# Optimization experiments

Measured on AMD Instinct MI355X. Metric: run time of the kernel, lower is better.

The kernel has to match this reference:

```python
import jax, jax.numpy as jnp
import numpy as np

N_NODES = 512      # nodes in the original graph
N_SUB = 512        # NodeDeleted -> one subgraph per node
E_SUB = 2097152    # edges in the union-of-subgraphs graph (avg degree 8)
E_ORIG = 8192      # edges in the original graph
IN_DIM = 64
EMB = 64
L = 4
TASKS = 10


def setup_inputs() -> dict:
    key = jax.random.key(0)
    ks = jax.random.split(key, 16)
    NT = N_NODES * N_SUB
    x = jax.random.normal(ks[0], (NT, IN_DIM), jnp.float32)
    # edges stay within a subgraph: global id = subgraph_id * N + local id
    eg = jax.random.randint(ks[1], (E_SUB,), 0, N_SUB)
    src = jax.random.randint(ks[2], (E_SUB,), 0, N_NODES)
    dst = jax.random.randint(ks[3], (E_SUB,), 0, N_NODES)
    edge_index = jnp.stack([eg * N_NODES + src, eg * N_NODES + dst]).astype(jnp.int32)
    original_edge_index = jax.random.randint(ks[4], (2, E_ORIG), 0, N_NODES).astype(jnp.int32)
    subgraph_node_idx = jnp.tile(jnp.arange(N_NODES, dtype=jnp.int32), N_SUB)
    subgraph_batch = jnp.repeat(jnp.arange(N_SUB, dtype=jnp.int32), N_NODES)
    p = lambda k, shape: jax.random.normal(k, shape, jnp.float32) * 0.05
    return dict(
        x=x,
        Wrel=p(ks[5], (L, EMB, IN_DIM)), brel=jnp.zeros((L, EMB), jnp.float32),
        Wroot=p(ks[6], (L, EMB, IN_DIM)),
        bn_gamma=jnp.ones((L, EMB), jnp.float32), bn_beta=jnp.zeros((L, EMB), jnp.float32),
        Wrel_s=p(ks[7], (L, EMB, IN_DIM)), brel_s=jnp.zeros((L, EMB), jnp.float32),
        Wroot_s=p(ks[8], (L, EMB, IN_DIM)),
        bns_gamma=jnp.ones((L, EMB), jnp.float32), bns_beta=jnp.zeros((L, EMB), jnp.float32),
        W1=p(ks[9], (2 * EMB, EMB)), b1=jnp.zeros((2 * EMB,), jnp.float32),
        W2=p(ks[10], (TASKS, 2 * EMB)), b2=jnp.zeros((TASKS,), jnp.float32),
        edge_index=edge_index, original_edge_index=original_edge_index,
        subgraph_node_idx=subgraph_node_idx, subgraph_batch=subgraph_batch,
        num_nodes_int=N_NODES,
    )


def _gconv(h, ei, Wr, br, Wt, n):
    # PyG GraphConv, aggr='add': lin_rel(sum_{j->i} x_j) + lin_root(x_i)
    agg = jax.ops.segment_sum(h[ei[0]], ei[1], num_segments=n)
    return agg @ Wr.T + br + h @ Wt.T


def _bn(h, g, b):
    # BatchNorm1d, training mode: biased batch stats, eps=1e-5
    mu = h.mean(0)
    var = ((h - mu) ** 2).mean(0)
    return (h - mu) * jax.lax.rsqrt(var + 1e-5) * g + b


def _smean(src, idx, n):
    s = jax.ops.segment_sum(src, idx, num_segments=n)
    c = jax.ops.segment_sum(jnp.ones((src.shape[0], 1), src.dtype), idx, num_segments=n)
    return s / jnp.maximum(c, 1.0)


def reference(x, Wrel, brel, Wroot, bn_gamma, bn_beta, Wrel_s, brel_s, Wroot_s,
              bns_gamma, bns_beta, W1, b1, W2, b2,
              edge_index, original_edge_index, subgraph_node_idx, subgraph_batch,
              num_nodes_int):
    N = num_nodes_int
    NT = x.shape[0]
    S = NT // N  # num_subgraphs
    h = x
    for i in range(Wrel.shape[0]):
        h1 = _bn(_gconv(h, edge_index, Wrel[i], brel[i], Wroot[i], NT),
                 bn_gamma[i], bn_beta[i])
        x_sum = _smean(h, subgraph_node_idx, N)              # [N, emb]
        h2 = _bn(_gconv(x_sum, original_edge_index, Wrel_s[i], brel_s[i], Wroot_s[i], N),
                 bns_gamma[i], bns_beta[i])
        h = jax.nn.relu(h1 + jnp.tile(h2, (S, 1)))           # broadcast h2 to every subgraph
    x_nodes = _smean(h, subgraph_node_idx, N)                # [N, emb]
    z = jax.nn.log_softmax(x_nodes, axis=-1)                 # log_softmax BEFORE final MLP (as in source)
    out = jax.nn.relu(z @ W1.T + b1) @ W2.T + b2             # [N, num_tasks]
    return out
```

## Files before the change

### kernel.cpp

```cpp
#include <hip/hip_runtime.h>
#include <math.h>

#define NT 262144
#define NS 512
#define ES 2097152
#define EO 8192
#define NLAYER 4
#define WROW 68
#define BSL 704
#define EREG 8192

typedef short bf16x8 __attribute__((ext_vector_type(8)));
typedef float f32x4 __attribute__((ext_vector_type(4)));

__device__ __forceinline__ void cvt_hilo(const float* v, bf16x8* hi, bf16x8* lo) {
    union U { bf16x8 v; unsigned u[4]; };
    U H, L;
    #pragma unroll
    for (int q = 0; q < 4; q++) {
        float v0 = v[2 * q], v1 = v[2 * q + 1];
        unsigned h01;
        asm("v_cvt_pk_bf16_f32 %0, %1, %2" : "=v"(h01) : "v"(v0), "v"(v1));
        float l0 = v0 - __uint_as_float(h01 << 16);
        float l1 = v1 - __uint_as_float(h01 & 0xffff0000u);
        unsigned l01;
        asm("v_cvt_pk_bf16_f32 %0, %1, %2" : "=v"(l01) : "v"(l0), "v"(l1));
        H.u[q] = h01; L.u[q] = l01;
    }
    *hi = H.v; *lo = L.v;
}

__global__ __launch_bounds__(256) void bucket_kernel(const int* __restrict__ ei,
        int* __restrict__ gcur, unsigned* __restrict__ rbuf) {
    __shared__ int lcnt[512];
    __shared__ int lcur[512];
    int p = blockIdx.x;
    int g = p & 7;
    int base = p * 4096;
    int tid = threadIdx.x;
    for (int t = tid; t < 512; t += 256) lcnt[t] = 0;
    __syncthreads();
    int subs[16];
    unsigned recs[16];
    #pragma unroll
    for (int j = 0; j < 16; j++) {
        int e = base + j * 256 + tid;
        int d = ei[ES + e];
        int srcl = ei[e] & 511;
        subs[j] = d >> 9;
        recs[j] = (unsigned)srcl | ((unsigned)(d & 511) << 16);
        atomicAdd(&lcnt[subs[j]], 1);
    }
    __syncthreads();
    for (int t = tid; t < 512; t += 256) {
        int c = lcnt[t];
        lcur[t] = c ? atomicAdd(&gcur[g * 512 + t], c) : 0;
    }
    __syncthreads();
    #pragma unroll
    for (int j = 0; j < 16; j++) {
        int s = subs[j];
        int pos = atomicAdd(&lcur[s], 1);
        if (pos < BSL) rbuf[((size_t)s * 8 + g) * BSL + pos] = recs[j];
    }
}

__global__ __launch_bounds__(512) void csr_sub_kernel(const int* __restrict__ gcur,
        const unsigned* __restrict__ rbuf, int* __restrict__ rowptr,
        unsigned short* __restrict__ ebuf) {
    __shared__ int sdeg[512];
    __shared__ int sscan[512];
    __shared__ int scur[512];
    __shared__ unsigned short erow[EREG];
    __shared__ int scnt[8];
    int s = blockIdx.x;
    int t = threadIdx.x;
    sdeg[t] = 0;
    if (t < 8) scnt[t] = min(gcur[t * 512 + s], BSL);
    unsigned* e32 = (unsigned*)erow;
    #pragma unroll
    for (int j = 0; j < 8; j++) e32[j * 512 + t] = 0x02000200u;
    __syncthreads();
    for (int g = 0; g < 8; g++) {
        int cg = scnt[g];
        const unsigned* rb = rbuf + ((size_t)s * 8 + g) * BSL;
        for (int i = t; i < cg; i += 512) atomicAdd(&sdeg[rb[i] >> 16], 1);
    }
    __syncthreads();
    int pdeg = (sdeg[t] + 3) & ~3;
    sscan[t] = pdeg;
    __syncthreads();
    for (int off = 1; off < 512; off <<= 1) {
        int x = (t >= off) ? sscan[t - off] : 0;
        __syncthreads();
        sscan[t] += x;
        __syncthreads();
    }
    int excl = sscan[t] - pdeg;
    scur[t] = excl;
    rowptr[s * 513 + t] = s * EREG + excl;
    if (t == 511) rowptr[s * 513 + 512] = s * EREG + sscan[511];
    __syncthreads();
    for (int g = 0; g < 8; g++) {
        int cg = scnt[g];
        const unsigned* rb = rbuf + ((size_t)s * 8 + g) * BSL;
        for (int i = t; i < cg; i += 512) {
            unsigned rec = rb[i];
            int pos = atomicAdd(&scur[rec >> 16], 1);
            erow[pos] = (unsigned short)(rec & 511);
        }
    }
    __syncthreads();
    uint4* eo = (uint4*)(ebuf + (size_t)s * EREG);
    const uint4* ei4 = (const uint4*)erow;
    eo[t] = ei4[t];
    eo[t + 512] = ei4[t + 512];
}

__global__ void small_csr_kernel(const int* __restrict__ oei, int* __restrict__ rowptrS,
                                 int* __restrict__ srcsS) {
    __shared__ int sdeg[NS];
    __shared__ int scur[NS];
    int t = threadIdx.x;
    if (t < NS) sdeg[t] = 0;
    __syncthreads();
    for (int e = t; e < EO; e += 1024) atomicAdd(&sdeg[oei[EO + e]], 1);
    __syncthreads();
    int myv = (t < NS) ? sdeg[t] : 0;
    __syncthreads();
    for (int off = 1; off < NS; off <<= 1) {
        int x = (t >= off && t < NS) ? sdeg[t - off] : 0;
        __syncthreads();
        if (t < NS) sdeg[t] += x;
        __syncthreads();
    }
    if (t < NS) {
        int excl = sdeg[t] - myv;
        rowptrS[t] = excl;
        scur[t] = excl;
        if (t == 0) rowptrS[NS] = EO;
    }
    __syncthreads();
    for (int e = t; e < EO; e += 1024) {
        int d = oei[EO + e];
        int pos = atomicAdd(&scur[d], 1);
        srcsS[pos] = oei[e];
    }
}

__global__ __launch_bounds__(512, 2) void gconv_sub_kernel(
    const float* __restrict__ hsrc,
    const float* __restrict__ h2,
    const float* __restrict__ stB, const float* __restrict__ stS,
    const float* __restrict__ gB, const float* __restrict__ bB,
    const float* __restrict__ gS, const float* __restrict__ bS,
    int mode,
    const int* __restrict__ rowptr, const unsigned short* __restrict__ ebuf,
    const float* __restrict__ Wr, const float* __restrict__ Wt,
    const float* __restrict__ br,
    float* __restrict__ hout, float* __restrict__ stats,
    const float* __restrict__ xsumIn, const int* __restrict__ rowptrS,
    const int* __restrict__ srcsS, const float* __restrict__ WrS,
    const float* __restrict__ WtS, const float* __restrict__ brS,
    float* __restrict__ h2out, float* __restrict__ statsS)
{
    extern __shared__ char smem[];
    int tid = threadIdx.x;

    if (blockIdx.x < 16) {
        float* wrt = (float*)smem;
        float* wtt = wrt + 4096;
        float4* aggT = (float4*)(wtt + 4096);
        float4* hT = aggT + 8 * 64;
        float* sbuf = (float*)(hT + 8 * 64);
        float* qbuf = sbuf + 512;
        float* brs = qbuf + 512;
        int b2 = blockIdx.x;

        for (int idx = tid; idx < 4096; idx += 512) {
            int cc = idx >> 6, kk = idx & 63;
            wrt[kk * 64 + ((kk + cc) & 63)] = WrS[idx];
            wtt[kk * 64 + ((kk + cc) & 63)] = WtS[idx];
        }
        if (tid < 64) brs[tid] = brS[tid];
        __syncthreads();

        int w = tid >> 6;
        int c = tid & 63;
        int node0 = (b2 * 8 + w) * 4;

        float* aggp = (float*)&aggT[w * 64];
        float* hp   = (float*)&hT[w * 64];
        #pragma unroll
        for (int r = 0; r < 4; r++) {
            int node = node0 + r;
            hp[c * 4 + r] = xsumIn[node * 64 + c];
            int e0 = rowptrS[node], e1 = rowptrS[node + 1];
            float a = 0.f;
            int e = e0;
            for (; e + 4 <= e1; e += 4) {
                int s0 = srcsS[e], s1 = srcsS[e + 1], s2 = srcsS[e + 2], s3 = srcsS[e + 3];
                float v0 = xsumIn[s0 * 64 + c];
                float v1 = xsumIn[s1 * 64 + c];
                float v2 = xsumIn[s2 * 64 + c];
                float v3 = xsumIn[s3 * 64 + c];
                a += (v0 + v1) + (v2 + v3);
            }
            for (; e < e1; e++) a += xsumIn[srcsS[e] * 64 + c];
            aggp[c * 4 + r] = a;
        }

        float o0 = brs[c], o1 = o0, o2 = o0, o3 = o0;
        #pragma unroll 8
        for (int k = 0; k < 64; k++) {
            float wr = wrt[k * 64 + ((k + c) & 63)];
            float wt = wtt[k * 64 + ((k + c) & 63)];
            float4 av = aggT[w * 64 + k];
            float4 hv = hT[w * 64 + k];
            o0 += wr * av.x + wt * hv.x;
            o1 += wr * av.y + wt * hv.y;
            o2 += wr * av.z + wt * hv.z;
            o3 += wr * av.w + wt * hv.w;
        }
        h2out[(node0 + 0) * 64 + c] = o0;
        h2out[(node0 + 1) * 64 + c] = o1;
        h2out[(node0 + 2) * 64 + c] = o2;
        h2out[(node0 + 3) * 64 + c] = o3;

        sbuf[w * 64 + c] = (o0 + o1) + (o2 + o3);
        qbuf[w * 64 + c] = (o0 * o0 + o1 * o1) + (o2 * o2 + o3 * o3);
        __syncthreads();
        int rep = b2 & 31;
        if (w == 0) {
            float s = 0.f;
            #pragma unroll
            for (int ww = 0; ww < 8; ww++) s += sbuf[ww * 64 + c];
            atomicAdd(&statsS[rep * 128 + c], s);
        } else if (w == 1) {
            float q = 0.f;
            #pragma unroll
            for (int ww = 0; ww < 8; ww++) q += qbuf[ww * 64 + c];
            atomicAdd(&statsS[rep * 128 + 64 + c], q);
        }
        return;
    }

    float* Wn = (float*)smem;
    float* bnp = Wn + 513 * WROW;

    int p = blockIdx.x - 16;
    int sub = p;
    int w = tid >> 6;
    int l = tid & 63;
    int cl = l & 15;
    int kg = l >> 4;
    int kg8 = kg * 8;
    int half = w >> 2;
    int m = w & 3;

    if (mode) {
        if (tid < 64) {
            int c = tid;
            float sb = 0.f, qb = 0.f, ss = 0.f, qs = 0.f;
            for (int r2 = 0; r2 < 32; r2++) {
                sb += stB[r2 * 128 + c];
                qb += stB[r2 * 128 + 64 + c];
                ss += stS[r2 * 128 + c];
                qs += stS[r2 * 128 + 64 + c];
            }
            float muB = sb * (1.f / 262144.f);
            float varB = qb * (1.f / 262144.f) - muB * muB;
            float scB = gB[c] * rsqrtf(varB + 1e-5f);
            bnp[c] = scB;
            bnp[64 + c] = bB[c] - muB * scB;
            float muS = ss * (1.f / 512.f);
            float varS = qs * (1.f / 512.f) - muS * muS;
            float scS = gS[c] * rsqrtf(varS + 1e-5f);
            bnp[128 + c] = scS;
            bnp[192 + c] = bS[c] - muS * scS;
        }
        __syncthreads();
    }

    const float* srcbase = hsrc + (size_t)sub * 512 * 64;
    for (int idx = tid; idx < 512 * 16; idx += 512) {
        int r = idx >> 4;
        int c4 = (idx & 15) * 4;
        float4 a = *(const float4*)(srcbase + r * 64 + c4);
        if (mode) {
            float4 b = *(const float4*)(h2 + r * 64 + c4);
            float4 sB4 = *(const float4*)(bnp + c4);
            float4 hB4 = *(const float4*)(bnp + 64 + c4);
            float4 sS4 = *(const float4*)(bnp + 128 + c4);
            float4 hS4 = *(const float4*)(bnp + 192 + c4);
            a.x = fmaxf(a.x * sB4.x + hB4.x + b.x * sS4.x + hS4.x, 0.f);
            a.y = fmaxf(a.y * sB4.y + hB4.y + b.y * sS4.y + hS4.y, 0.f);
            a.z = fmaxf(a.z * sB4.z + hB4.z + b.z * sS4.z + hS4.z, 0.f);
            a.w = fmaxf(a.w * sB4.w + hB4.w + b.w * sS4.w + hS4.w, 0.f);
        }
        *(float4*)(Wn + r * WROW + c4) = a;
    }
    if (tid < WROW) Wn[512 * WROW + tid] = 0.f;

    bf16x8 Bh[16], Bl[16];
    float bias0, bias1, bias2, bias3;
    #pragma unroll
    for (int c = 0; c < 4; c++) {
        int col = c * 16 + cl;
        #pragma unroll
        for (int ch = 0; ch < 4; ch++) {
            const float* mat = (ch < 2) ? Wr : Wt;
            int k = (ch & 1) * 32 + kg8;
            float vv[8];
            *(float4*)vv = *(const float4*)(mat + col * 64 + k);
            *(float4*)(vv + 4) = *(const float4*)(mat + col * 64 + k + 4);
            cvt_hilo(vv, &Bh[c * 4 + ch], &Bl[c * 4 + ch]);
        }
    }
    bias0 = br[cl];
    bias1 = br[16 + cl];
    bias2 = br[32 + cl];
    bias3 = br[48 + cl];

    const uint2* ebuf2 = (const uint2*)ebuf;
    __syncthreads();

#define GATH1(qv) { \
        const float* pp = Wn + (qv) * WROW + kg8; \
        float4 tg0 = *(const float4*)(pp); \
        float4 tg1 = *(const float4*)(pp + 4); \
        float4 tg2 = *(const float4*)(pp + 32); \
        float4 tg3 = *(const float4*)(pp + 36); \
        a0.x += tg0.x; a0.y += tg0.y; a0.z += tg0.z; a0.w += tg0.w; \
        a1.x += tg1.x; a1.y += tg1.y; a1.z += tg1.z; a1.w += tg1.w; \
        a2.x += tg2.x; a2.y += tg2.y; a2.z += tg2.z; a2.w += tg2.w; \
        a3.x += tg3.x; a3.y += tg3.y; a3.z += tg3.z; a3.w += tg3.w; \
    }

#define DO_CHUNK(g0h, g1h, ch) { \
        float gg[8]; \
        *(float4*)gg = g0h; *(float4*)(gg + 4) = g1h; \
        bf16x8 ah, al; \
        cvt_hilo(gg, &ah, &al); \
        acc0 = __builtin_amdgcn_mfma_f32_16x16x32_bf16(ah, Bh[0 * 4 + ch], acc0, 0, 0, 0); \
        acc1 = __builtin_amdgcn_mfma_f32_16x16x32_bf16(ah, Bh[1 * 4 + ch], acc1, 0, 0, 0); \
        acc2 = __builtin_amdgcn_mfma_f32_16x16x32_bf16(ah, Bh[2 * 4 + ch], acc2, 0, 0, 0); \
        acc3 = __builtin_amdgcn_mfma_f32_16x16x32_bf16(ah, Bh[3 * 4 + ch], acc3, 0, 0, 0); \
        acc0 = __builtin_amdgcn_mfma_f32_16x16x32_bf16(al, Bh[0 * 4 + ch], acc0, 0, 0, 0); \
        acc1 = __builtin_amdgcn_mfma_f32_16x16x32_bf16(al, Bh[1 * 4 + ch], acc1, 0, 0, 0); \
        acc2 = __builtin_amdgcn_mfma_f32_16x16x32_bf16(al, Bh[2 * 4 + ch], acc2, 0, 0, 0); \
        acc3 = __builtin_amdgcn_mfma_f32_16x16x32_bf16(al, Bh[3 * 4 + ch], acc3, 0, 0, 0); \
        acc0 = __builtin_amdgcn_mfma_f32_16x16x32_bf16(ah, Bl[0 * 4 + ch], acc0, 0, 0, 0); \
        acc1 = __builtin_amdgcn_mfma_f32_16x16x32_bf16(ah, Bl[1 * 4 + ch], acc1, 0, 0, 0); \
        acc2 = __builtin_amdgcn_mfma_f32_16x16x32_bf16(ah, Bl[2 * 4 + ch], acc2, 0, 0, 0); \
        acc3 = __builtin_amdgcn_mfma_f32_16x16x32_bf16(ah, Bl[3 * 4 + ch], acc3, 0, 0, 0); \
    }

    float s0 = 0.f, s1 = 0.f, s2 = 0.f, s3 = 0.f;
    float q0s = 0.f, q1s = 0.f, q2s = 0.f, q3s = 0.f;

    for (int tt = 0; tt < 4; tt++) {
        int tile = half * 4 + tt;
        int nb = sub * 512 + tile * 64;
        int row = tile * 64 + m * 16 + cl;
        int rpb = sub * 513;
        int e0q = rowptr[rpb + row] >> 2;
        int e1q = rowptr[rpb + row + 1] >> 2;

        float4 a0 = make_float4(0.f, 0.f, 0.f, 0.f);
        float4 a1 = a0, a2 = a0, a3 = a0;
        uint2 rr = make_uint2(0u, 0u);
        int u = e0q;
        if (u < e1q) rr = ebuf2[u];
        while (u < e1q) {
            uint2 cur = rr;
            ++u;
            if (u < e1q) rr = ebuf2[u];
            unsigned q0 = cur.x & 0xffffu;
            unsigned q1 = cur.x >> 16;
            unsigned q2 = cur.y & 0xffffu;
            unsigned q3 = cur.y >> 16;
            GATH1(q0);
            GATH1(q1);
            GATH1(q2);
            GATH1(q3);
        }

        const float* wrow = Wn + (size_t)(tile * 64 + m * 16 + cl) * WROW + kg8;
        float4 r0 = *(const float4*)(wrow);
        float4 r1 = *(const float4*)(wrow + 4);
        float4 r2 = *(const float4*)(wrow + 32);
        float4 r3 = *(const float4*)(wrow + 36);

        f32x4 acc0, acc1, acc2, acc3;
        #pragma unroll
        for (int j = 0; j < 4; j++) {
            acc0[j] = bias0; acc1[j] = bias1; acc2[j] = bias2; acc3[j] = bias3;
        }
        DO_CHUNK(a0, a1, 0);
        DO_CHUNK(a2, a3, 1);
        DO_CHUNK(r0, r1, 2);
        DO_CHUNK(r2, r3, 3);

        int node0 = nb + m * 16 + kg * 4;
        #pragma unroll
        for (int j = 0; j < 4; j++) {
            float v0 = acc0[j], v1 = acc1[j], v2 = acc2[j], v3 = acc3[j];
            size_t rowb = (size_t)(node0 + j) * 64;
            hout[rowb + cl] = v0;
            hout[rowb + 16 + cl] = v1;
            hout[rowb + 32 + cl] = v2;
            hout[rowb + 48 + cl] = v3;
            s0 += v0; q0s += v0 * v0;
            s1 += v1; q1s += v1 * v1;
            s2 += v2; q2s += v2 * v2;
            s3 += v3; q3s += v3 * v3;
        }
    }

    s0 += __shfl_xor(s0, 16, 64); s0 += __shfl_xor(s0, 32, 64);
    s1 += __shfl_xor(s1, 16, 64); s1 += __shfl_xor(s1, 32, 64);
    s2 += __shfl_xor(s2, 16, 64); s2 += __shfl_xor(s2, 32, 64);
    s3 += __shfl_xor(s3, 16, 64); s3 += __shfl_xor(s3, 32, 64);
    q0s += __shfl_xor(q0s, 16, 64); q0s += __shfl_xor(q0s, 32, 64);
    q1s += __shfl_xor(q1s, 16, 64); q1s += __shfl_xor(q1s, 32, 64);
    q2s += __shfl_xor(q2s, 16, 64); q2s += __shfl_xor(q2s, 32, 64);
    q3s += __shfl_xor(q3s, 16, 64); q3s += __shfl_xor(q3s, 32, 64);
    if (kg == 0) {
        int rep = p & 31;
        atomicAdd(&stats[rep * 128 + cl], s0);
        atomicAdd(&stats[rep * 128 + 16 + cl], s1);
        atomicAdd(&stats[rep * 128 + 32 + cl], s2);
        atomicAdd(&stats[rep * 128 + 48 + cl], s3);
        atomicAdd(&stats[rep * 128 + 64 + cl], q0s);
        atomicAdd(&stats[rep * 128 + 80 + cl], q1s);
        atomicAdd(&stats[rep * 128 + 96 + cl], q2s);
        atomicAdd(&stats[rep * 128 + 112 + cl], q3s);
    }
#undef GATH1
#undef DO_CHUNK
}

__global__ __launch_bounds__(1024) void xsum_kernel(
    const float* __restrict__ hsrc, const float* __restrict__ h2,
    const float* __restrict__ stB, const float* __restrict__ stS,
    const float* __restrict__ gB, const float* __restrict__ bB,
    const float* __restrict__ gS, const float* __restrict__ bS,
    int mode, float* __restrict__ xsum)
{
    __shared__ float bnp[256];
    __shared__ float red[16][64];
    int t = threadIdx.x;
    if (mode) {
        if (t < 64) {
            int c = t;
            float sb = 0.f, qb = 0.f, ss = 0.f, qs = 0.f;
            for (int r2 = 0; r2 < 32; r2++) {
                sb += stB[r2 * 128 + c];
                qb += stB[r2 * 128 + 64 + c];
                ss += stS[r2 * 128 + c];
                qs += stS[r2 * 128 + 64 + c];
            }
            float muB = sb * (1.f / 262144.f);
            float varB = qb * (1.f / 262144.f) - muB * muB;
            float scB = gB[c] * rsqrtf(varB + 1e-5f);
            bnp[c] = scB;
            bnp[64 + c] = bB[c] - muB * scB;
            float muS = ss * (1.f / 512.f);
            float varS = qs * (1.f / 512.f) - muS * muS;
            float scS = gS[c] * rsqrtf(varS + 1e-5f);
            bnp[128 + c] = scS;
            bnp[192 + c] = bS[c] - muS * scS;
        }
        __syncthreads();
    }

    int w = t >> 6;
    int l = t & 63;
    int c4 = (l & 15) * 4;
    int r = l >> 4;
    int n = blockIdx.x;

    float bx = 0.f, by = 0.f, bz = 0.f, bw = 0.f;
    float4 sB = make_float4(1.f, 1.f, 1.f, 1.f);
    float4 hB = make_float4(0.f, 0.f, 0.f, 0.f);
    if (mode) {
        sB = *(const float4*)(bnp + c4);
        hB = *(const float4*)(bnp + 64 + c4);
        float4 sS = *(const float4*)(bnp + 128 + c4);
        float4 hS = *(const float4*)(bnp + 192 + c4);
        float4 b2 = *(const float4*)(h2 + n * 64 + c4);
        bx = b2.x * sS.x + hS.x;
        by = b2.y * sS.y + hS.y;
        bz = b2.z * sS.z + hS.z;
        bw = b2.w * sS.w + hS.w;
    }

    float4 acc = make_float4(0.f, 0.f, 0.f, 0.f);
    #pragma unroll
    for (int j = 0; j < 8; j++) {
        int si = w * 32 + j * 4 + r;
        size_t base = (size_t)(si * 512 + n) * 64 + c4;
        float4 a = *(const float4*)(hsrc + base);
        float4 v;
        if (mode) {
            v.x = fmaxf(a.x * sB.x + hB.x + bx, 0.f);
            v.y = fmaxf(a.y * sB.y + hB.y + by, 0.f);
            v.z = fmaxf(a.z * sB.z + hB.z + bz, 0.f);
            v.w = fmaxf(a.w * sB.w + hB.w + bw, 0.f);
        } else {
            v = a;
        }
        acc.x += v.x; acc.y += v.y; acc.z += v.z; acc.w += v.w;
    }
    acc.x += __shfl_xor(acc.x, 16, 64); acc.y += __shfl_xor(acc.y, 16, 64);
    acc.z += __shfl_xor(acc.z, 16, 64); acc.w += __shfl_xor(acc.w, 16, 64);
    acc.x += __shfl_xor(acc.x, 32, 64); acc.y += __shfl_xor(acc.y, 32, 64);
    acc.z += __shfl_xor(acc.z, 32, 64); acc.w += __shfl_xor(acc.w, 32, 64);
    if (l < 16) {
        red[w][c4 + 0] = acc.x;
        red[w][c4 + 1] = acc.y;
        red[w][c4 + 2] = acc.z;
        red[w][c4 + 3] = acc.w;
    }
    __syncthreads();
    if (t < 64) {
        float tot = 0.f;
        #pragma unroll
        for (int ww = 0; ww < 16; ww++) tot += red[ww][t];
        xsum[n * 64 + t] = tot * (1.f / 512.f);
    }
}

__global__ void head_kernel(const float* __restrict__ xs, const float* __restrict__ W1,
                            const float* __restrict__ b1, const float* __restrict__ W2,
                            const float* __restrict__ b2, float* __restrict__ out) {
    __shared__ float z[64];
    __shared__ float hid[128];
    int t = threadIdx.x;
    int n = blockIdx.x;
    if (t < 64) {
        float v = xs[n * 64 + t];
        float m = v;
        for (int off = 32; off >= 1; off >>= 1) m = fmaxf(m, __shfl_xor(m, off, 64));
        float e = expf(v - m);
        float s = e;
        for (int off = 32; off >= 1; off >>= 1) s += __shfl_xor(s, off, 64);
        z[t] = v - m - logf(s);
    }
    __syncthreads();
    {
        float acc = b1[t];
        const float* wrow = W1 + t * 64;
        #pragma unroll 8
        for (int k = 0; k < 64; k++) acc += z[k] * wrow[k];
        hid[t] = fmaxf(acc, 0.f);
    }
    __syncthreads();
    if (t < 10) {
        float o = b2[t];
        const float* wrow = W2 + t * 128;
        #pragma unroll 8
        for (int j = 0; j < 128; j++) o += hid[j] * wrow[j];
        out[n * 10 + t] = o;
    }
}

extern "C" void kernel_launch(void* const* d_in, const int* in_sizes, int n_in,
                              void* d_out, int out_size, void* d_ws, size_t ws_size,
                              hipStream_t stream) {
    const float* x       = (const float*)d_in[0];
    const float* Wrel    = (const float*)d_in[1];
    const float* brel    = (const float*)d_in[2];
    const float* Wroot   = (const float*)d_in[3];
    const float* bn_g    = (const float*)d_in[4];
    const float* bn_b    = (const float*)d_in[5];
    const float* Wrel_s  = (const float*)d_in[6];
    const float* brel_s  = (const float*)d_in[7];
    const float* Wroot_s = (const float*)d_in[8];
    const float* bns_g   = (const float*)d_in[9];
    const float* bns_b   = (const float*)d_in[10];
    const float* W1      = (const float*)d_in[11];
    const float* b1      = (const float*)d_in[12];
    const float* W2      = (const float*)d_in[13];
    const float* b2      = (const float*)d_in[14];
    const int* ei        = (const int*)d_in[15];
    const int* oei       = (const int*)d_in[16];
    float* out = (float*)d_out;

    char* ws = (char*)d_ws;
    size_t off = 0;
    auto alloc = [&](size_t bytes) -> void* {
        void* p = ws + off;
        off = (off + bytes + 255) & ~(size_t)255;
        return p;
    };
    float* h1    = (float*)alloc((size_t)NT * 64 * 4);
    float* xsum  = (float*)alloc(NS * 64 * 4);
    float* h2buf = (float*)alloc((size_t)2 * NS * 64 * 4);
    float* stats = (float*)alloc(NLAYER * 2 * 4096 * 4);
    int* rowptr  = (int*)alloc((size_t)NS * 513 * 4);
    int* gcur    = (int*)alloc(8 * 512 * 4);
    unsigned short* ebuf = (unsigned short*)alloc((size_t)NS * EREG * 2);
    int* rowptrS = (int*)alloc(513 * 4);
    int* srcsS   = (int*)alloc(EO * 4);
    unsigned* rbuf = (unsigned*)h1;
    (void)ws_size; (void)in_sizes; (void)n_in; (void)out_size;

    hipMemsetAsync(gcur, 0, 8 * 512 * 4, stream);
    hipMemsetAsync(stats, 0, (size_t)NLAYER * 2 * 4096 * 4, stream);

    bucket_kernel<<<ES / 4096, 256, 0, stream>>>(ei, gcur, rbuf);
    csr_sub_kernel<<<NS, 512, 0, stream>>>(gcur, rbuf, rowptr, ebuf);
    small_csr_kernel<<<1, 1024, 0, stream>>>(oei, rowptrS, srcsS);

    const size_t SMEM = (513 * WROW + 256) * 4;

    for (int i = 0; i < NLAYER; i++) {
        int mode = (i > 0);
        const float* hsrc = mode ? h1 : x;
        const float* h2R = h2buf + (size_t)((i - 1) & 1) * NS * 64;
        float* h2W = h2buf + (size_t)(i & 1) * NS * 64;
        const float* stPB = stats + (i - 1) * 8192;
        const float* stPS = stPB + 4096;
        const float* gBp = bn_g + (i - 1) * 64;
        const float* bBp = bn_b + (i - 1) * 64;
        const float* gSp = bns_g + (i - 1) * 64;
        const float* bSp = bns_b + (i - 1) * 64;
        float* stB = stats + i * 8192;
        float* stS = stB + 4096;

        xsum_kernel<<<NS, 1024, 0, stream>>>(hsrc, h2R, stPB, stPS, gBp, bBp, gSp, bSp,
                                             mode, xsum);
        gconv_sub_kernel<<<NS + 16, 512, SMEM, stream>>>(hsrc, h2R, stPB, stPS,
            gBp, bBp, gSp, bSp, mode, rowptr, ebuf,
            Wrel + i * 4096, Wroot + i * 4096, brel + i * 64, h1, stB,
            xsum, rowptrS, srcsS,
            Wrel_s + i * 4096, Wroot_s + i * 4096, brel_s + i * 64, h2W, stS);
    }
    {
        const float* stPB = stats + 3 * 8192;
        const float* stPS = stPB + 4096;
        const float* h2R = h2buf + (size_t)(3 & 1) * NS * 64;
        xsum_kernel<<<NS, 1024, 0, stream>>>(h1, h2R, stPB, stPS,
            bn_g + 3 * 64, bn_b + 3 * 64, bns_g + 3 * 64, bns_b + 3 * 64, 1, xsum);
    }
    head_kernel<<<NS, 128, 0, stream>>>(xsum, W1, b1, W2, b2, out);
}
```

Baseline: 546.0 us.

## Fold small-graph gconv into main subgraph blocks, pre-transpose small weights once

The 16 extra blocks that computed the original-graph GraphConv per layer are removed. Instead, wave 0 of each of the 512 subgraph blocks computes one original-graph node's output after finishing its main work, using warp shuffles and weights transposed once up front in small_csr_kernel. This removes the tail imbalance and the per-block shared-memory weight staging of the 16 special blocks. The cost is a serial gather-and-matvec tail on one wave per block, plus a global atomic per channel for every node.

New measurement: 554.5 us. Within noise of the previous version (+1.6%).

```diff
diff --git a/kernel.cpp b/kernel.cpp
--- a/kernel.cpp
+++ b/kernel.cpp
@@ -118,7 +118,10 @@
 }
 
 __global__ void small_csr_kernel(const int* __restrict__ oei, int* __restrict__ rowptrS,
-                                 int* __restrict__ srcsS) {
+                                 int* __restrict__ srcsS,
+                                 const float* __restrict__ Wrel_s,
+                                 const float* __restrict__ Wroot_s,
+                                 float* __restrict__ WrT, float* __restrict__ WtT) {
     __shared__ int sdeg[NS];
     __shared__ int scur[NS];
     int t = threadIdx.x;
@@ -145,6 +148,13 @@
         int d = oei[EO + e];
         int pos = atomicAdd(&scur[d], 1);
         srcsS[pos] = oei[e];
+    }
+    for (int idx = t; idx < NLAYER * 4096; idx += 1024) {
+        int layer = idx >> 12;
+        int rem = idx & 4095;
+        int cc = rem >> 6, kk = rem & 63;
+        WrT[layer * 4096 + kk * 64 + cc] = Wrel_s[idx];
+        WtT[layer * 4096 + kk * 64 + cc] = Wroot_s[idx];
     }
 }
 
@@ -160,95 +170,17 @@
     const float* __restrict__ br,
     float* __restrict__ hout, float* __restrict__ stats,
     const float* __restrict__ xsumIn, const int* __restrict__ rowptrS,
-    const int* __restrict__ srcsS, const float* __restrict__ WrS,
-    const float* __restrict__ WtS, const float* __restrict__ brS,
+    const int* __restrict__ srcsS, const float* __restrict__ WrT,
+    const float* __restrict__ WtT, const float* __restrict__ brS,
     float* __restrict__ h2out, float* __restrict__ statsS)
 {
     extern __shared__ char smem[];
     int tid = threadIdx.x;
 
-    if (blockIdx.x < 16) {
-        float* wrt = (float*)smem;
-        float* wtt = wrt + 4096;
-        float4* aggT = (float4*)(wtt + 4096);
-        float4* hT = aggT + 8 * 64;
-        float* sbuf = (float*)(hT + 8 * 64);
-        float* qbuf = sbuf + 512;
-        float* brs = qbuf + 512;
-        int b2 = blockIdx.x;
-
-        for (int idx = tid; idx < 4096; idx += 512) {
-            int cc = idx >> 6, kk = idx & 63;
-            wrt[kk * 64 + ((kk + cc) & 63)] = WrS[idx];
-            wtt[kk * 64 + ((kk + cc) & 63)] = WtS[idx];
-        }
-        if (tid < 64) brs[tid] = brS[tid];
-        __syncthreads();
-
-        int w = tid >> 6;
-        int c = tid & 63;
-        int node0 = (b2 * 8 + w) * 4;
-
-        float* aggp = (float*)&aggT[w * 64];
-        float* hp   = (float*)&hT[w * 64];
-        #pragma unroll
-        for (int r = 0; r < 4; r++) {
-            int node = node0 + r;
-            hp[c * 4 + r] = xsumIn[node * 64 + c];
-            int e0 = rowptrS[node], e1 = rowptrS[node + 1];
-            float a = 0.f;
-            int e = e0;
-            for (; e + 4 <= e1; e += 4) {
-                int s0 = srcsS[e], s1 = srcsS[e + 1], s2 = srcsS[e + 2], s3 = srcsS[e + 3];
-                float v0 = xsumIn[s0 * 64 + c];
-                float v1 = xsumIn[s1 * 64 + c];
-                float v2 = xsumIn[s2 * 64 + c];
-                float v3 = xsumIn[s3 * 64 + c];
-                a += (v0 + v1) + (v2 + v3);
-            }
-            for (; e < e1; e++) a += xsumIn[srcsS[e] * 64 + c];
-            aggp[c * 4 + r] = a;
-        }
-
-        float o0 = brs[c], o1 = o0, o2 = o0, o3 = o0;
-        #pragma unroll 8
-        for (int k = 0; k < 64; k++) {
-            float wr = wrt[k * 64 + ((k + c) & 63)];
-            float wt = wtt[k * 64 + ((k + c) & 63)];
-            float4 av = aggT[w * 64 + k];
-            float4 hv = hT[w * 64 + k];
-            o0 += wr * av.x + wt * hv.x;
-            o1 += wr * av.y + wt * hv.y;
-            o2 += wr * av.z + wt * hv.z;
-            o3 += wr * av.w + wt * hv.w;
-        }
-        h2out[(node0 + 0) * 64 + c] = o0;
-        h2out[(node0 + 1) * 64 + c] = o1;
-        h2out[(node0 + 2) * 64 + c] = o2;
-        h2out[(node0 + 3) * 64 + c] = o3;
-
-        sbuf[w * 64 + c] = (o0 + o1) + (o2 + o3);
-        qbuf[w * 64 + c] = (o0 * o0 + o1 * o1) + (o2 * o2 + o3 * o3);
-        __syncthreads();
-        int rep = b2 & 31;
-        if (w == 0) {
-            float s = 0.f;
-            #pragma unroll
-            for (int ww = 0; ww < 8; ww++) s += sbuf[ww * 64 + c];
-            atomicAdd(&statsS[rep * 128 + c], s);
-        } else if (w == 1) {
-            float q = 0.f;
-            #pragma unroll
-            for (int ww = 0; ww < 8; ww++) q += qbuf[ww * 64 + c];
-            atomicAdd(&statsS[rep * 128 + 64 + c], q);
-        }
-        return;
-    }
-
     float* Wn = (float*)smem;
     float* bnp = Wn + 513 * WROW;
 
-    int p = blockIdx.x - 16;
+    int p = blockIdx.x;
     int sub = p;
     int w = tid >> 6;
     int l = tid & 63;
@@ -436,6 +368,25 @@
         atomicAdd(&stats[rep * 128 + 80 + cl], q1s);
         atomicAdd(&stats[rep * 128 + 96 + cl], q2s);
         atomicAdd(&stats[rep * 128 + 112 + cl], q3s);
+    }
+
+    if (w == 0) {
+        int c = l;
+        float agg = 0.f;
+        int e0 = rowptrS[p], e1 = rowptrS[p + 1];
+        for (int e = e0; e < e1; e++) agg += xsumIn[srcsS[e] * 64 + c];
+        float own = xsumIn[p * 64 + c];
+        float o = brS[c];
+        #pragma unroll 4
+        for (int k = 0; k < 64; k++) {
+            float ak = __shfl(agg, k, 64);
+            float hk = __shfl(own, k, 64);
+            o += WrT[k * 64 + c] * ak + WtT[k * 64 + c] * hk;
+        }
+        h2out[p * 64 + c] = o;
+        int rep = p & 31;
+        atomicAdd(&statsS[rep * 128 + c], o);
+        atomicAdd(&statsS[rep * 128 + 64 + c], o * o);
     }
 #undef GATH1
 #undef DO_CHUNK
@@ -604,6 +555,8 @@
     unsigned short* ebuf = (unsigned short*)alloc((size_t)NS * EREG * 2);
     int* rowptrS = (int*)alloc(513 * 4);
     int* srcsS   = (int*)alloc(EO * 4);
+    float* wrTs  = (float*)alloc(NLAYER * 4096 * 4);
+    float* wtTs  = (float*)alloc(NLAYER * 4096 * 4);
     unsigned* rbuf = (unsigned*)h1;
     (void)ws_size; (void)in_sizes; (void)n_in; (void)out_size;
 
@@ -612,7 +565,8 @@
 
     bucket_kernel<<<ES / 4096, 256, 0, stream>>>(ei, gcur, rbuf);
     csr_sub_kernel<<<NS, 512, 0, stream>>>(gcur, rbuf, rowptr, ebuf);
-    small_csr_kernel<<<1, 1024, 0, stream>>>(oei, rowptrS, srcsS);
+    small_csr_kernel<<<1, 1024, 0, stream>>>(oei, rowptrS, srcsS,
+                                             Wrel_s, Wroot_s, wrTs, wtTs);
 
     const size_t SMEM = (513 * WROW + 256) * 4;
 
@@ -632,11 +586,11 @@
 
         xsum_kernel<<<NS, 1024, 0, stream>>>(hsrc, h2R, stPB, stPS, gBp, bBp, gSp, bSp,
                                              mode, xsum);
-        gconv_sub_kernel<<<NS + 16, 512, SMEM, stream>>>(hsrc, h2R, stPB, stPS,
+        gconv_sub_kernel<<<NS, 512, SMEM, stream>>>(hsrc, h2R, stPB, stPS,
             gBp, bBp, gSp, bSp, mode, rowptr, ebuf,
             Wrel + i * 4096, Wroot + i * 4096, brel + i * 64, h1, stB,
             xsum, rowptrS, srcsS,
-            Wrel_s + i * 4096, Wroot_s + i * 4096, brel_s + i * 64, h2W, stS);
+            wrTs + i * 4096, wtTs + i * 4096, brel_s + i * 64, h2W, stS);
     }
     {
         const float* stPB = stats + 3 * 8192;
```
